# Performance work log

Hardware: AMD Instinct MI355X
Metric: run time of the kernel (lower is better)

## Reference

```python
import jax, jax.numpy as jnp
import numpy as np

L = 4096   # num_tokens (one prefill sequence)
D = 2048   # hidden_size
HK = 16    # num_k_heads
HV = 32    # num_v_heads
DK = 128   # head_k_dim
DV = 128   # head_v_dim
RATIO = HV // HK
EPS = 1e-6


def setup_inputs() -> dict:
    key = jax.random.key(0)
    ks = jax.random.split(key, 11)
    s = 0.02
    return {
        "hidden_states": jax.random.normal(ks[0], (L, D), jnp.float32),
        "Wq": jax.random.normal(ks[1], (D, HK * DK), jnp.float32) * s,
        "Wk": jax.random.normal(ks[2], (D, HK * DK), jnp.float32) * s,
        "Wv": jax.random.normal(ks[3], (D, HV * DV), jnp.float32) * s,
        "Wz": jax.random.normal(ks[4], (D, HV * DV), jnp.float32) * s,
        "Wb": jax.random.normal(ks[5], (D, HV), jnp.float32) * s,
        "Wa": jax.random.normal(ks[6], (D, HV), jnp.float32) * s,
        "A_log": jnp.log(jax.random.uniform(ks[7], (HV,), jnp.float32, 1.0, 16.0)),
        "dt_bias": jax.random.normal(ks[8], (HV,), jnp.float32) * 0.5,
        "norm_weight": jnp.ones((DV,), jnp.float32),
        "W_out": jax.random.normal(ks[9], (HV * DV, D), jnp.float32) * s,
    }


def _l2norm(x):
    return x * jax.lax.rsqrt(jnp.sum(x * x, axis=-1, keepdims=True) + EPS)


def reference(hidden_states, Wq, Wk, Wv, Wz, Wb, Wa, A_log, dt_bias, norm_weight, W_out):
    h = hidden_states
    # --- input projections (qkvz + ba split) ---
    q = _l2norm((h @ Wq).reshape(L, HK, DK))            # [L, HK, DK]
    k = _l2norm((h @ Wk).reshape(L, HK, DK))
    v = (h @ Wv).reshape(L, HV, DV)                     # [L, HV, DV]
    z = (h @ Wz).reshape(L, HV, DV)                     # gate for RMSNorm
    beta = jax.nn.sigmoid(h @ Wb)                       # [L, HV]
    g = -jnp.exp(A_log) * jax.nn.softplus(h @ Wa + dt_bias)  # [L, HV]
    decay = jnp.exp(g)                                  # per-token per-head decay
    # repeat shared q/k heads to value heads (GQA ratio)
    q = jnp.repeat(q, RATIO, axis=1) * (DK ** -0.5)     # [L, HV, DK]
    k = jnp.repeat(k, RATIO, axis=1)

    # --- gated delta rule recurrence over tokens ---
    def step(S, xs):
        q_t, k_t, v_t, b_t, d_t = xs                    # [HV,DK],[HV,DK],[HV,DV],[HV],[HV]
        S = S * d_t[:, None, None]                      # decay state [HV, DK, DV]
        pred = jnp.einsum('hk,hkv->hv', k_t, S)         # memory readout
        delta = (v_t - pred) * b_t[:, None]             # delta-rule correction
        S = S + k_t[:, :, None] * delta[:, None, :]
        o = jnp.einsum('hk,hkv->hv', q_t, S)
        return S, o

    S0 = jnp.zeros((HV, DK, DV), jnp.float32)
    _, core = jax.lax.scan(step, S0, (q, k, v, beta, decay))  # core: [L, HV, DV]

    # --- gated RMSNorm: x * silu(z), rms-normalize over head dim ---
    x = core * jax.nn.silu(z)
    x = x * jax.lax.rsqrt(jnp.mean(x * x, axis=-1, keepdims=True) + EPS) * norm_weight

    # --- output projection ---
    return x.reshape(L, HV * DV) @ W_out                # [L, D]
```

## Files before the change

kernel.cpp:

```cpp
#include <hip/hip_runtime.h>

#define LTOK 4096
#define DHID 2048
#define HKN  16
#define HVN  32
#define DKK  128
#define NTOT 12288

typedef unsigned short u16;
typedef __attribute__((ext_vector_type(8))) short short8;
typedef __attribute__((ext_vector_type(8))) unsigned short u16x8;
typedef __attribute__((ext_vector_type(4))) unsigned short u16x4;
typedef __attribute__((ext_vector_type(4))) float f32x4;

__device__ __forceinline__ float b2f(u16 u) {
  unsigned int x = ((unsigned int)u) << 16;
  return __builtin_bit_cast(float, x);
}
__device__ __forceinline__ u16 f2bf(float f) {
  unsigned int u = __builtin_bit_cast(unsigned int, f);
  u += 0x7FFFu + ((u >> 16) & 1u);
  return (u16)(u >> 16);
}

template<int C> __device__ __forceinline__ float dppmv(float x) {
  int i = __builtin_amdgcn_update_dpp(0, __builtin_bit_cast(int, x), C, 0xF, 0xF, true);
  return __builtin_bit_cast(float, i);
}
__device__ __forceinline__ float red16(float x) {
  x += dppmv<0xB1>(x);
  x += dppmv<0x4E>(x);
  x += dppmv<0x124>(x);
  x += dppmv<0x128>(x);
  return x;
}

__device__ __forceinline__ void gld16(const void* g, void* l) {
  __builtin_amdgcn_global_load_lds((const __attribute__((address_space(1))) void*)g,
                                   (__attribute__((address_space(3))) void*)l, 16, 0, 0);
}

template<int OFF> __device__ __forceinline__ short8 dsr(unsigned a) {
  short8 r;
  asm volatile("ds_read_b128 %0, %1 offset:%2" : "=v"(r) : "v"(a), "n"(OFF));
  return r;
}

__device__ __forceinline__ int sw16(int r, int c, int rowc) { return (r * rowc + c) ^ ((r & 7) << 3); }

__device__ __forceinline__ void cstore(u16* C, size_t i, float v) { C[i] = f2bf(v); }
__device__ __forceinline__ void cstore(float* C, size_t i, float v) { C[i] = v; }

__global__ __launch_bounds__(256)
void k_cvt(const float* __restrict__ s, u16* __restrict__ d, int n) {
  const int i = (blockIdx.x * 256 + threadIdx.x) * 4;
  const float4 v = *(const float4*)(s + i);
  ushort4 o;
  o.x = f2bf(v.x); o.y = f2bf(v.y); o.z = f2bf(v.z); o.w = f2bf(v.w);
  *(ushort4*)(d + i) = o;
}

__global__ __launch_bounds__(256)
void k_tr(const float* __restrict__ src, u16* __restrict__ dst, int R, int C) {
  __shared__ float tl[32][33];
  const int r0 = blockIdx.y * 32, c0 = blockIdx.x * 32;
  const int tr = threadIdx.x >> 3, tc = (threadIdx.x & 7) * 4;
  const float4 v = *(const float4*)(src + (size_t)(r0 + tr) * C + c0 + tc);
  tl[tr][tc] = v.x; tl[tr][tc + 1] = v.y; tl[tr][tc + 2] = v.z; tl[tr][tc + 3] = v.w;
  __syncthreads();
  ushort4 o;
  o.x = f2bf(tl[tc + 0][tr]); o.y = f2bf(tl[tc + 1][tr]);
  o.z = f2bf(tl[tc + 2][tr]); o.w = f2bf(tl[tc + 3][tr]);
  *(ushort4*)(dst + (size_t)(c0 + tr) * R + r0 + tc) = o;
}

#define MFMA16(a, b, c) __builtin_amdgcn_mfma_f32_16x16x32_bf16(a, b, c, 0, 0, 0)

template<typename OutT, int NWN>
__global__ __launch_bounds__(512, 2)
void k_g256(const u16* __restrict__ A, const u16* __restrict__ Bt, OutT* __restrict__ C,
            int M, int N, int K, int NT) {
  constexpr int BUFE = 8192 + NWN * 2048;
  constexpr int BN = NWN * 64;
  __shared__ u16 Lds[4 * BUFE];
  const int tid = threadIdx.x;
  const int lane = tid & 63, w = tid >> 6;
  const int fr = lane & 15, fq = lane >> 4;
  const int wm = (w >> 2) * 128, wn = (w & 3) * (NWN * 16);
  const int nkt = K >> 5;
  const size_t sK = (size_t)K;

  const int MT = gridDim.x / NT;
  const int nts = (NT < 16) ? NT : 16;
  const int per_super = MT * nts;
  const int super = blockIdx.x / per_super;
  const int within = blockIdx.x % per_super;
  const int mtg = MT >> 3;
  const int q = within >> 3;
  const int mt = (within & 7) * mtg + (q % mtg);
  const int nt = super * nts + q / mtg;

  const int kslot = ((tid & 3) ^ ((tid >> 3) & 3)) * 8;
  const u16* aS = A + (size_t)(mt * 256 + (tid >> 2)) * sK + kslot;
  const u16* bS = Bt + (size_t)(nt * BN + (tid >> 2)) * sK + kslot;

  f32x4 acc[8][NWN] = {};

  auto STAGE = [&](int kt_) {
    const int sk = (kt_ < nkt) ? kt_ : nkt - 1;
    u16* base = &Lds[(kt_ & 3) * BUFE];
    gld16(aS + (size_t)sk * 32, base + w * 512);
    gld16(aS + 128 * sK + (size_t)sk * 32, base + w * 512 + 4096);
    gld16(bS + (size_t)sk * 32, base + 8192 + w * 512);
    if constexpr (NWN == 4)
      gld16(bS + 128 * sK + (size_t)sk * 32, base + 8192 + w * 512 + 4096);
  };

  STAGE(0); STAGE(1); STAGE(2);

  const int akey = (fr >> 1) & 3;
  const unsigned ldsBase = (unsigned)(size_t)(__attribute__((address_space(3))) void*)&Lds[0];
  const unsigned aA0 = ldsBase + 2u * (unsigned)((wm + fr) * 32 + ((fq ^ akey) << 3));
  const unsigned bA0 = ldsBase + 2u * (unsigned)(8192 + (wn + fr) * 32 + ((fq ^ akey) << 3));

  for (int kt = 0; kt < nkt; ++kt) {
    if constexpr (NWN == 4) asm volatile("s_waitcnt vmcnt(8)" ::: "memory");
    else                    asm volatile("s_waitcnt vmcnt(6)" ::: "memory");
    __builtin_amdgcn_s_barrier();
    __builtin_amdgcn_sched_barrier(0);
    STAGE(kt + 3);
    const unsigned bo = (unsigned)((kt & 3) * BUFE * 2);
    const unsigned aA = aA0 + bo, bA = bA0 + bo;
    short8 af[8], bf[NWN];
    bf[0] = dsr<0>(bA); bf[1] = dsr<1024>(bA);
    if constexpr (NWN == 4) { bf[2] = dsr<2048>(bA); bf[3] = dsr<3072>(bA); }
    af[0] = dsr<0>(aA);    af[1] = dsr<1024>(aA);
    af[2] = dsr<2048>(aA); af[3] = dsr<3072>(aA);
    af[4] = dsr<4096>(aA); af[5] = dsr<5120>(aA);
    af[6] = dsr<6144>(aA); af[7] = dsr<7168>(aA);
    asm volatile("s_waitcnt lgkmcnt(6)" ::: "memory");
    __builtin_amdgcn_sched_barrier(0);
    __builtin_amdgcn_s_setprio(1);
#pragma unroll
    for (int j = 0; j < NWN; ++j) { acc[0][j] = MFMA16(af[0], bf[j], acc[0][j]);
                                    acc[1][j] = MFMA16(af[1], bf[j], acc[1][j]); }
    asm volatile("s_waitcnt lgkmcnt(4)" ::: "memory");
    __builtin_amdgcn_sched_barrier(0);
#pragma unroll
    for (int j = 0; j < NWN; ++j) { acc[2][j] = MFMA16(af[2], bf[j], acc[2][j]);
                                    acc[3][j] = MFMA16(af[3], bf[j], acc[3][j]); }
    asm volatile("s_waitcnt lgkmcnt(2)" ::: "memory");
    __builtin_amdgcn_sched_barrier(0);
#pragma unroll
    for (int j = 0; j < NWN; ++j) { acc[4][j] = MFMA16(af[4], bf[j], acc[4][j]);
                                    acc[5][j] = MFMA16(af[5], bf[j], acc[5][j]); }
    asm volatile("s_waitcnt lgkmcnt(0)" ::: "memory");
    __builtin_amdgcn_sched_barrier(0);
#pragma unroll
    for (int j = 0; j < NWN; ++j) { acc[6][j] = MFMA16(af[6], bf[j], acc[6][j]);
                                    acc[7][j] = MFMA16(af[7], bf[j], acc[7][j]); }
    __builtin_amdgcn_s_setprio(0);
  }

  const int r0 = mt * 256 + wm + fq * 4;
  const int c0 = nt * BN + wn + fr;
#pragma unroll
  for (int i = 0; i < 8; ++i)
#pragma unroll
    for (int j = 0; j < NWN; ++j)
#pragma unroll
      for (int e = 0; e < 4; ++e)
        cstore(C, (size_t)(r0 + i * 16 + e) * N + c0 + j * 16, acc[i][j][e]);
}

__global__ __launch_bounds__(256)
void k_ba(const float* __restrict__ h, const float* __restrict__ Wb, const float* __restrict__ Wa,
          const float* __restrict__ A_log, const float* __restrict__ dtb,
          float* __restrict__ beta, float* __restrict__ g_out) {
  const int w = threadIdx.x >> 6, lane = threadIdx.x & 63;
  const int t = blockIdx.x * 4 + w;
  const int j = lane & 31;
  const bool isB = lane < 32;
  const float* __restrict__ hr = h + (size_t)t * DHID;
  const float* Wc = isB ? Wb : Wa;
  float acc = 0.f;
  for (int kk = 0; kk < DHID; ++kk) acc = fmaf(hr[kk], Wc[(size_t)kk * HVN + j], acc);
  if (isB) {
    beta[(size_t)t * HVN + j] = 1.f / (1.f + expf(-acc));
  } else {
    float xx = acc + dtb[j];
    float sp = (xx > 20.f) ? xx : log1pf(expf(xx));
    g_out[(size_t)t * HVN + j] = -expf(A_log[j]) * sp;
  }
}

__global__ __launch_bounds__(256)
void k_l2n(u16* __restrict__ qkvz) {
  const int w = threadIdx.x >> 6, lane = threadIdx.x & 63;
  const int r = blockIdx.x * 4 + w;
  const int isK = r >> 16;
  const int rr = r & 65535;
  const int t = rr >> 4, hd = rr & 15;
  u16* p = qkvz + (size_t)t * NTOT + isK * 2048 + hd * DKK + lane * 2;
  float a = b2f(p[0]), b = b2f(p[1]);
  float ss = a * a + b * b;
  ss = red16(ss);
  ss += __shfl_xor(ss, 16);
  ss += __shfl_xor(ss, 32);
  const float sc = rsqrtf(ss + 1e-6f) * (isK ? 1.f : 0.08838834764831845f);
  p[0] = f2bf(a * sc); p[1] = f2bf(b * sc);
}

__global__ __launch_bounds__(256)
void k_r1(const u16* __restrict__ qkvz, const float* __restrict__ beta_g,
          const float* __restrict__ g_g, u16* __restrict__ UM_g, float* __restrict__ cumL_g) {
  const int pair = blockIdx.x;
  const int hv = pair >> 6, n = pair & 63;
  const int hk = hv >> 1;
  const int t0 = n * 64;
  const int tid = threadIdx.x, lane = tid & 63, wv = tid >> 6;
  const int fr = lane & 15, fq = lane >> 4;

  __shared__ __align__(16) u16 Xb[256 * 64];
  __shared__ __align__(16) u16 Dbuf0[64 * 64 * 2];
  __shared__ __align__(16) u16 Dbuf1[64 * 64 * 2];
  __shared__ float Lc[64];
  __shared__ float Bc[64];
  u16* Kl = Dbuf0;

  const int j = tid & 63, h = tid >> 6;
  const u16* kg = qkvz + (size_t)(t0 + j) * NTOT + 2048 + hk * DKK + h * 32;
  const u16* vg = qkvz + (size_t)(t0 + j) * NTOT + 4096 + hv * DKK + h * 32;
  u16x8 kv[4], vv[4];
#pragma unroll
  for (int i = 0; i < 4; ++i) { kv[i] = *(const u16x8*)(kg + i * 8); vv[i] = *(const u16x8*)(vg + i * 8); }
  if (tid < 64) {
    Lc[tid] = g_g[(size_t)(t0 + tid) * HVN + hv];
    Bc[tid] = beta_g[(size_t)(t0 + tid) * HVN + hv];
  }
#pragma unroll
  for (int i = 0; i < 4; ++i) *(u16x8*)&Kl[sw16(j, h * 32 + i * 8, 128)] = kv[i];
  __syncthreads();
  if (tid == 0) { float a = 0.f; for (int t = 0; t < 64; ++t) { a += Lc[t]; Lc[t] = a; } }
  __syncthreads();
  if (tid < 64) cumL_g[(size_t)pair * 64 + tid] = Lc[tid];

  {
    const float bj = Bc[j];
    const float mj = bj * __expf(Lc[j]);
#pragma unroll
    for (int i = 0; i < 4; ++i)
#pragma unroll
      for (int e = 0; e < 8; ++e) {
        int c = h * 32 + i * 8 + e;
        Xb[sw16(c, j, 64)] = f2bf(bj * b2f(vv[i][e]));
        Xb[sw16(128 + c, j, 64)] = f2bf(mj * b2f(kv[i][e]));
      }
  }
  f32x4 kk[4] = {};
#pragma unroll
  for (int ks = 0; ks < 4; ++ks) {
    short8 afr = *(const short8*)&Kl[sw16(wv * 16 + fr, ks * 32 + fq * 8, 128)];
#pragma unroll
    for (int ct = 0; ct < 4; ++ct) {
      short8 bfr = *(const short8*)&Kl[sw16(ct * 16 + fr, ks * 32 + fq * 8, 128)];
      kk[ct] = MFMA16(afr, bfr, kk[ct]);
    }
  }
  __syncthreads();

  f32x4 acc[16];
#pragma unroll
  for (int ct = 0; ct < 16; ++ct) {
    u16x4 xi = *(const u16x4*)&Xb[sw16(ct * 16 + fr, wv * 16 + fq * 4, 64)];
    acc[ct][0] = b2f(xi[0]); acc[ct][1] = b2f(xi[1]); acc[ct][2] = b2f(xi[2]); acc[ct][3] = b2f(xi[3]);
  }
#pragma unroll
  for (int ct = 0; ct < 4; ++ct) {
    const int s = ct * 16 + fr;
    u16x4 pk;
#pragma unroll
    for (int e = 0; e < 4; ++e) {
      const int t = wv * 16 + fq * 4 + e;
      float v = (s < t) ? -Bc[t] * __expf(Lc[t] - Lc[s]) * kk[ct][e] : 0.f;
      pk[e] = f2bf(v);
      Dbuf0[sw16(t, s, 64)] = pk[e];
    }
    *(u16x4*)&Dbuf0[4096 + sw16(s, wv * 16 + fq * 4, 64)] = pk;
  }
  __syncthreads();

  u16* DA = Dbuf0;
  u16* DB = Dbuf1;
  for (int stg = 0; stg < 6; ++stg) {
    u16* Dr = DA;
    u16* Dc = DA + 4096;
    short8 da0 = *(const short8*)&Dr[sw16(wv * 16 + fr, 0 + fq * 8, 64)];
    short8 da1 = *(const short8*)&Dr[sw16(wv * 16 + fr, 32 + fq * 8, 64)];
#pragma unroll
    for (int ct = 0; ct < 16; ++ct) {
      short8 b0 = *(const short8*)&Xb[sw16(ct * 16 + fr, 0 + fq * 8, 64)];
      short8 b1 = *(const short8*)&Xb[sw16(ct * 16 + fr, 32 + fq * 8, 64)];
      acc[ct] = MFMA16(da0, b0, acc[ct]);
      acc[ct] = MFMA16(da1, b1, acc[ct]);
    }
    f32x4 sq[4] = {};
    if (stg < 5) {
#pragma unroll
      for (int ct = 0; ct < 4; ++ct) {
        short8 sb0 = *(const short8*)&Dc[sw16(ct * 16 + fr, 0 + fq * 8, 64)];
        short8 sb1 = *(const short8*)&Dc[sw16(ct * 16 + fr, 32 + fq * 8, 64)];
        sq[ct] = MFMA16(da0, sb0, sq[ct]);
        sq[ct] = MFMA16(da1, sb1, sq[ct]);
      }
    }
    __syncthreads();
#pragma unroll
    for (int ct = 0; ct < 16; ++ct) {
      u16x4 pk;
      pk[0] = f2bf(acc[ct][0]); pk[1] = f2bf(acc[ct][1]); pk[2] = f2bf(acc[ct][2]); pk[3] = f2bf(acc[ct][3]);
      *(u16x4*)&Xb[sw16(ct * 16 + fr, wv * 16 + fq * 4, 64)] = pk;
    }
    if (stg < 5) {
#pragma unroll
      for (int ct = 0; ct < 4; ++ct) {
        u16x4 pk;
        pk[0] = f2bf(sq[ct][0]); pk[1] = f2bf(sq[ct][1]); pk[2] = f2bf(sq[ct][2]); pk[3] = f2bf(sq[ct][3]);
        *(u16x4*)&(DB + 4096)[sw16(ct * 16 + fr, wv * 16 + fq * 4, 64)] = pk;
#pragma unroll
        for (int e = 0; e < 4; ++e) DB[sw16(wv * 16 + fq * 4 + e, ct * 16 + fr, 64)] = pk[e];
      }
    }
    __syncthreads();
    u16* tmp = DA; DA = DB; DB = tmp;
  }

#pragma unroll
  for (int ct = 0; ct < 16; ++ct) {
    const int c = ct * 16 + fr;
#pragma unroll
    for (int e = 0; e < 4; ++e) {
      const int t = wv * 16 + fq * 4 + e;
      float v = acc[ct][e];
      if (ct >= 8) v = -v;
      UM_g[((size_t)pair * 64 + t) * 256 + c] = f2bf(v);
    }
  }
}

__global__ __launch_bounds__(512)
void k_r2(u16* __restrict__ qkvz, const u16* __restrict__ UM_g,
          const float* __restrict__ cumL_g, u16* __restrict__ o1_g) {
  const int hv = blockIdx.x >> 1, cs = blockIdx.x & 1;
  const int hk = hv >> 1;
  const int tid = threadIdx.x, lane = tid & 63, w = tid >> 6;
  const int fr = lane & 15, fq = lane >> 4;
  const int j = tid & 63, h = tid >> 6;

  __shared__ __align__(16) u16 Ml2[2][8192];
  __shared__ __align__(16) u16 Ql2[2][8192];
  __shared__ __align__(16) u16 Kt2[2][8192];
  __shared__ __align__(16) u16 Ul2[2][4096];
  __shared__ __align__(16) u16 dT[4096];
  __shared__ __align__(16) u16 SbT[8192];
  __shared__ __align__(16) u16 o1b[4096];
  __shared__ float Lc2[2][64];

  const int tw = w & 3;
  const int d0 = (w >> 2) * 2;

  f32x4 sacc[4];
#pragma unroll
  for (int d = 0; d < 4; ++d) sacc[d] = (f32x4){0.f, 0.f, 0.f, 0.f};
  for (int i = tid; i < 8192; i += 512) SbT[i] = 0;

  u16x8 pQ0, pQ1, pK0, pK1, pM0, pM1, pU0;
  float pL, pL63;

#define PREF(nn) {                                                            \
    const int nc = ((nn) < 64) ? (nn) : 63;                                   \
    const int pr = hv * 64 + nc; const int tt0 = nc * 64;                     \
    const u16* qg = qkvz + (size_t)(tt0 + j) * NTOT + hk * DKK + h * 16;      \
    pQ0 = *(const u16x8*)qg;          pQ1 = *(const u16x8*)(qg + 8);          \
    pK0 = *(const u16x8*)(qg + 2048); pK1 = *(const u16x8*)(qg + 2056);       \
    const u16* mg = UM_g + ((size_t)pr * 64 + j) * 256;                       \
    pM0 = *(const u16x8*)(mg + 128 + h * 16);                                 \
    pM1 = *(const u16x8*)(mg + 136 + h * 16);                                 \
    pU0 = *(const u16x8*)(mg + cs * 64 + h * 8);                              \
    pL = cumL_g[(size_t)pr * 64 + j]; pL63 = cumL_g[(size_t)pr * 64 + 63]; }

#define STW(b) {                                                              \
    *(u16x8*)&Ql2[b][sw16(j, h * 16, 128)] = pQ0;                             \
    *(u16x8*)&Ql2[b][sw16(j, h * 16 + 8, 128)] = pQ1;                         \
    *(u16x8*)&Ml2[b][sw16(j, h * 16, 128)] = pM0;                             \
    *(u16x8*)&Ml2[b][sw16(j, h * 16 + 8, 128)] = pM1;                         \
    const float scK = __expf(pL63 - pL);                                      \
    _Pragma("unroll")                                                         \
    for (int e = 0; e < 8; ++e) {                                             \
      Kt2[b][sw16(h * 16 + e, j, 64)] = f2bf(scK * b2f(pK0[e]));              \
      Kt2[b][sw16(h * 16 + 8 + e, j, 64)] = f2bf(scK * b2f(pK1[e]));          \
      Ul2[b][sw16(h * 8 + e, j, 64)] = pU0[e];                                \
    }                                                                         \
    if (h == 0) Lc2[b][j] = pL; }

  PREF(0)
  STW(0)
  __syncthreads();

  for (int n = 0; n < 64; ++n) {
    const int cur = n & 1;
    const int pair = hv * 64 + n, t0 = n * 64;
    const float curL63 = pL63;
    PREF(n + 1)

    short8 amf[4], aqf[4];
#pragma unroll
    for (int ks = 0; ks < 4; ++ks) {
      amf[ks] = *(const short8*)&Ml2[cur][sw16(tw * 16 + fr, ks * 32 + fq * 8, 128)];
      aqf[ks] = *(const short8*)&Ql2[cur][sw16(tw * 16 + fr, ks * 32 + fq * 8, 128)];
    }
    float el[4];
#pragma unroll
    for (int e = 0; e < 4; ++e) el[e] = __expf(Lc2[cur][tw * 16 + fq * 4 + e]);
#pragma unroll
    for (int dd = 0; dd < 2; ++dd) {
      const int d = d0 + dd;
      u16x4 uv = *(const u16x4*)&Ul2[cur][sw16(d * 16 + fr, tw * 16 + fq * 4, 64)];
      f32x4 dc;
      dc[0] = b2f(uv[0]); dc[1] = b2f(uv[1]); dc[2] = b2f(uv[2]); dc[3] = b2f(uv[3]);
      f32x4 oc = {};
#pragma unroll
      for (int ks = 0; ks < 4; ++ks) {
        short8 bs = *(const short8*)&SbT[sw16(d * 16 + fr, ks * 32 + fq * 8, 128)];
        dc = MFMA16(amf[ks], bs, dc);
        oc = MFMA16(aqf[ks], bs, oc);
      }
      u16x4 pk;
      pk[0] = f2bf(dc[0]); pk[1] = f2bf(dc[1]); pk[2] = f2bf(dc[2]); pk[3] = f2bf(dc[3]);
      *(u16x4*)&dT[sw16(d * 16 + fr, tw * 16 + fq * 4, 64)] = pk;
#pragma unroll
      for (int e = 0; e < 4; ++e)
        o1b[sw16(tw * 16 + fq * 4 + e, d * 16 + fr, 64)] = f2bf(oc[e] * el[e]);
    }
    __syncthreads();

    {
      const int i = tid * 8;
      u16x8 vd = *(const u16x8*)&dT[i];
      const int f = cs * 4096 + i;
      *(u16x8*)(qkvz + (size_t)(t0 + (f >> 7)) * NTOT + 4096 + hv * DKK + (f & 127)) = vd;
      u16x8 vo = *(const u16x8*)&o1b[i];
      *(u16x8*)(o1_g + (size_t)pair * 8192 + (size_t)(i >> 6) * 128 + cs * 64 + (i & 63)) = vo;
    }
    STW(cur ^ 1)
    {
      const float eC = __expf(curL63);
      short8 ak0 = *(const short8*)&Kt2[cur][sw16(w * 16 + fr, fq * 8, 64)];
      short8 ak1 = *(const short8*)&Kt2[cur][sw16(w * 16 + fr, 32 + fq * 8, 64)];
#pragma unroll
      for (int d = 0; d < 4; ++d) {
        short8 bd0 = *(const short8*)&dT[sw16(d * 16 + fr, fq * 8, 64)];
        short8 bd1 = *(const short8*)&dT[sw16(d * 16 + fr, 32 + fq * 8, 64)];
        f32x4 sa = sacc[d];
#pragma unroll
        for (int e = 0; e < 4; ++e) sa[e] *= eC;
        sa = MFMA16(ak0, bd0, sa);
        sa = MFMA16(ak1, bd1, sa);
        sacc[d] = sa;
        u16x4 pk;
        pk[0] = f2bf(sa[0]); pk[1] = f2bf(sa[1]); pk[2] = f2bf(sa[2]); pk[3] = f2bf(sa[3]);
        *(u16x4*)&SbT[sw16(d * 16 + fr, w * 16 + fq * 4, 128)] = pk;
      }
    }
    __syncthreads();
  }
#undef PREF
#undef STW
}

__global__ __launch_bounds__(512)
void k_r3(const u16* __restrict__ qkvz, const u16* __restrict__ o1_g,
          const float* __restrict__ cumL_g, const float* __restrict__ nw,
          u16* __restrict__ x) {
  const int pair = blockIdx.x, hv = pair >> 6, n = pair & 63, hk = hv >> 1, t0 = n * 64;
  const int tid = threadIdx.x, lane = tid & 63, w = tid >> 6;
  const int fr = lane & 15, fq = lane >> 4;
  const int j = tid & 63, h = tid >> 6;

  __shared__ __align__(16) u16 Ql[8192];
  __shared__ __align__(16) u16 Kl[8192];
  __shared__ __align__(16) u16 Gl[4096];
  __shared__ __align__(16) u16 dTl[8192];
  __shared__ __align__(16) float of[64 * 132];
  __shared__ float Lc[64];
  __shared__ float Lw[128];

  {
    const u16* qg = qkvz + (size_t)(t0 + j) * NTOT + hk * DKK + h * 16;
    u16x8 q0 = *(const u16x8*)qg, q1 = *(const u16x8*)(qg + 8);
    u16x8 k0 = *(const u16x8*)(qg + 2048), k1 = *(const u16x8*)(qg + 2056);
    *(u16x8*)&Ql[sw16(j, h * 16, 128)] = q0;
    *(u16x8*)&Ql[sw16(j, h * 16 + 8, 128)] = q1;
    *(u16x8*)&Kl[sw16(j, h * 16, 128)] = k0;
    *(u16x8*)&Kl[sw16(j, h * 16 + 8, 128)] = k1;
  }
#pragma unroll
  for (int it = 0; it < 2; ++it) {
    const int f = ((w * 2 + it) * 64 + lane) * 8;
    gld16(qkvz + (size_t)(t0 + (f >> 7)) * NTOT + 4096 + hv * DKK + (f & 127),
          (char*)dTl + (w * 2 + it) * 1024);
  }
  if (tid < 64) Lc[tid] = cumL_g[(size_t)pair * 64 + tid];
  if (tid < 128) Lw[tid] = nw[tid];
  __syncthreads();

  const int tw = w & 3, sp = (w >> 2) * 2;
  {
    f32x4 kk0 = {}, kk1 = {};
#pragma unroll
    for (int ks = 0; ks < 4; ++ks) {
      short8 aq = *(const short8*)&Ql[sw16(tw * 16 + fr, ks * 32 + fq * 8, 128)];
      short8 b0 = *(const short8*)&Kl[sw16(sp * 16 + fr, ks * 32 + fq * 8, 128)];
      short8 b1 = *(const short8*)&Kl[sw16((sp + 1) * 16 + fr, ks * 32 + fq * 8, 128)];
      kk0 = MFMA16(aq, b0, kk0);
      kk1 = MFMA16(aq, b1, kk1);
    }
#pragma unroll
    for (int e = 0; e < 4; ++e) {
      const int t = tw * 16 + fq * 4 + e;
      const float Lt = Lc[t];
      const int s0 = sp * 16 + fr, s1 = s0 + 16;
      Gl[sw16(t, s0, 64)] = f2bf((s0 <= t) ? kk0[e] * __expf(Lt - Lc[s0]) : 0.f);
      Gl[sw16(t, s1, 64)] = f2bf((s1 <= t) ? kk1[e] * __expf(Lt - Lc[s1]) : 0.f);
    }
  }
  __syncthreads();

  {
    short8 ag0 = *(const short8*)&Gl[sw16(tw * 16 + fr, fq * 8, 64)];
    short8 ag1 = *(const short8*)&Gl[sw16(tw * 16 + fr, 32 + fq * 8, 64)];
#pragma unroll
    for (int dd = 0; dd < 4; ++dd) {
      const int d = (w >> 2) * 4 + dd;
      short8 bd0 = *(const short8*)&dTl[sw16(d * 16 + fr, fq * 8, 64)];
      short8 bd1 = *(const short8*)&dTl[sw16(d * 16 + fr, 32 + fq * 8, 64)];
      f32x4 oc = {};
      oc = MFMA16(ag0, bd0, oc);
      oc = MFMA16(ag1, bd1, oc);
#pragma unroll
      for (int e = 0; e < 4; ++e) of[(tw * 16 + fq * 4 + e) * 132 + d * 16 + fr] = oc[e];
    }
  }
  __syncthreads();

  {
    const int t = tid >> 3, q8 = tid & 7;
    const u16* zp = qkvz + (size_t)(t0 + t) * NTOT + 8192 + hv * DKK + q8 * 16;
    const u16* op = o1_g + (size_t)pair * 8192 + t * 128;
    float xv[16];
    float ss = 0.f;
#pragma unroll
    for (int i = 0; i < 2; ++i) {
      u16x8 zv = *(const u16x8*)(zp + i * 8);
      u16x8 ov = *(const u16x8*)(op + (((q8 * 16 + i * 8) ^ ((t & 7) << 3))));
#pragma unroll
      for (int e = 0; e < 8; ++e) {
        float z = b2f(zv[e]);
        float o = of[t * 132 + q8 * 16 + i * 8 + e] + b2f(ov[e]);
        float xx = o * (z / (1.f + __expf(-z)));
        xv[i * 8 + e] = xx;
        ss = fmaf(xx, xx, ss);
      }
    }
    ss += __shfl_xor(ss, 1);
    ss += __shfl_xor(ss, 2);
    ss += __shfl_xor(ss, 4);
    const float scl = rsqrtf(ss * (1.f / 128.f) + 1e-6f);
    u16* xo = x + (size_t)(t0 + t) * 4096 + hv * DKK + q8 * 16;
#pragma unroll
    for (int i = 0; i < 2; ++i) {
      u16x8 pk;
#pragma unroll
      for (int e = 0; e < 8; ++e) pk[e] = f2bf(xv[i * 8 + e] * scl * Lw[q8 * 16 + i * 8 + e]);
      *(u16x8*)(xo + i * 8) = pk;
    }
  }
}

extern "C" void kernel_launch(void* const* d_in, const int* in_sizes, int n_in,
                              void* d_out, int out_size, void* d_ws, size_t ws_size,
                              hipStream_t stream) {
  const float* h    = (const float*)d_in[0];
  const float* Wq   = (const float*)d_in[1];
  const float* Wk   = (const float*)d_in[2];
  const float* Wv   = (const float*)d_in[3];
  const float* Wz   = (const float*)d_in[4];
  const float* Wb   = (const float*)d_in[5];
  const float* Wa   = (const float*)d_in[6];
  const float* Alog = (const float*)d_in[7];
  const float* dtb  = (const float*)d_in[8];
  const float* nw   = (const float*)d_in[9];
  const float* Wo   = (const float*)d_in[10];
  char* ws = (char*)d_ws;
  u16* h_bf  = (u16*)(ws);
  u16* Wt    = (u16*)(ws + 16777216ull);
  u16* UM    = (u16*)(ws);
  u16* Wto   = (u16*)(ws + 67108864ull);
  u16* qkvz  = (u16*)(ws + 83886080ull);
  u16* o1g   = (u16*)(ws + 184549376ull);
  u16* xbuf  = (u16*)(ws + 16777216ull);
  float* beta  = (float*)(ws + 218103808ull);
  float* g     = (float*)(ws + 218103808ull + 524288ull);
  float* cumL  = (float*)(ws + 218103808ull + 1048576ull);

  k_cvt<<<8192, 256, 0, stream>>>(h, h_bf, LTOK * DHID);
  k_tr<<<dim3(64, 64), 256, 0, stream>>>(Wq, Wt, 2048, 2048);
  k_tr<<<dim3(64, 64), 256, 0, stream>>>(Wk, Wt + 2048ull * 2048, 2048, 2048);
  k_tr<<<dim3(128, 64), 256, 0, stream>>>(Wv, Wt + 4096ull * 2048, 2048, 4096);
  k_tr<<<dim3(128, 64), 256, 0, stream>>>(Wz, Wt + 8192ull * 2048, 2048, 4096);
  k_tr<<<dim3(64, 128), 256, 0, stream>>>(Wo, Wto, 4096, 2048);
  k_g256<u16, 4><<<768, 512, 0, stream>>>(h_bf, Wt, qkvz, 4096, 12288, 2048, 48);
  k_ba<<<1024, 256, 0, stream>>>(h, Wb, Wa, Alog, dtb, beta, g);
  k_l2n<<<32768, 256, 0, stream>>>(qkvz);
  k_r1<<<2048, 256, 0, stream>>>(qkvz, beta, g, UM, cumL);
  k_r2<<<64, 512, 0, stream>>>(qkvz, UM, cumL, o1g);
  k_r3<<<2048, 512, 0, stream>>>(qkvz, o1g, cumL, nw, xbuf);
  k_g256<float, 2><<<256, 512, 0, stream>>>(xbuf, Wto, (float*)d_out, 4096, 2048, 4096, 16);
}
```

Measured before the change: 831.3 us.

## Split sequential recurrence kernel across four value-column slices per head

```diff
diff --git a/kernel.cpp b/kernel.cpp
--- a/kernel.cpp
+++ b/kernel.cpp
@@ -351,30 +351,28 @@
 __global__ __launch_bounds__(512)
 void k_r2(u16* __restrict__ qkvz, const u16* __restrict__ UM_g,
           const float* __restrict__ cumL_g, u16* __restrict__ o1_g) {
-  const int hv = blockIdx.x >> 1, cs = blockIdx.x & 1;
+  const int hv = blockIdx.x >> 2, cs = blockIdx.x & 3;
   const int hk = hv >> 1;
   const int tid = threadIdx.x, lane = tid & 63, w = tid >> 6;
   const int fr = lane & 15, fq = lane >> 4;
   const int j = tid & 63, h = tid >> 6;
+  const int tw = w & 3, dwv = w >> 2;
 
   __shared__ __align__(16) u16 Ml2[2][8192];
   __shared__ __align__(16) u16 Ql2[2][8192];
   __shared__ __align__(16) u16 Kt2[2][8192];
-  __shared__ __align__(16) u16 Ul2[2][4096];
-  __shared__ __align__(16) u16 dT[4096];
-  __shared__ __align__(16) u16 SbT[8192];
-  __shared__ __align__(16) u16 o1b[4096];
+  __shared__ __align__(16) u16 dT[2048];
+  __shared__ __align__(16) u16 SbT[4096];
+  __shared__ __align__(16) u16 o1b[2048];
   __shared__ float Lc2[2][64];
 
-  const int tw = w & 3;
-  const int d0 = (w >> 2) * 2;
-
-  f32x4 sacc[4];
-#pragma unroll
-  for (int d = 0; d < 4; ++d) sacc[d] = (f32x4){0.f, 0.f, 0.f, 0.f};
-  for (int i = tid; i < 8192; i += 512) SbT[i] = 0;
-
-  u16x8 pQ0, pQ1, pK0, pK1, pM0, pM1, pU0;
+  f32x4 sacc[2];
+#pragma unroll
+  for (int d = 0; d < 2; ++d) sacc[d] = (f32x4){0.f, 0.f, 0.f, 0.f};
+  for (int i = tid; i < 4096; i += 512) SbT[i] = 0;
+
+  u16x8 pQ0, pQ1, pK0, pK1, pM0, pM1;
+  u16 pUn0, pUn1, pUn2, pUn3, pUc0, pUc1, pUc2, pUc3;
   float pL, pL63;
 
 #define PREF(nn) {                                                            \
@@ -386,7 +384,9 @@
     const u16* mg = UM_g + ((size_t)pr * 64 + j) * 256;                       \
     pM0 = *(const u16x8*)(mg + 128 + h * 16);                                 \
     pM1 = *(const u16x8*)(mg + 136 + h * 16);                                 \
-    pU0 = *(const u16x8*)(mg + cs * 64 + h * 8);                              \
+    const u16* ug = UM_g + ((size_t)pr * 64 + tw * 16 + fq * 4) * 256         \
+                    + cs * 32 + dwv * 16 + fr;                                \
+    pUn0 = ug[0]; pUn1 = ug[256]; pUn2 = ug[512]; pUn3 = ug[768];             \
     pL = cumL_g[(size_t)pr * 64 + j]; pL63 = cumL_g[(size_t)pr * 64 + 63]; }
 
 #define STW(b) {                                                              \
@@ -399,7 +399,6 @@
     for (int e = 0; e < 8; ++e) {                                             \
       Kt2[b][sw16(h * 16 + e, j, 64)] = f2bf(scK * b2f(pK0[e]));              \
       Kt2[b][sw16(h * 16 + 8 + e, j, 64)] = f2bf(scK * b2f(pK1[e]));          \
-      Ul2[b][sw16(h * 8 + e, j, 64)] = pU0[e];                                \
     }                                                                         \
     if (h == 0) Lc2[b][j] = pL; }
 
@@ -410,6 +409,7 @@
   for (int n = 0; n < 64; ++n) {
     const int cur = n & 1;
     const int pair = hv * 64 + n, t0 = n * 64;
+    pUc0 = pUn0; pUc1 = pUn1; pUc2 = pUn2; pUc3 = pUn3;
     const float curL63 = pL63;
     PREF(n + 1)
 
@@ -422,35 +422,33 @@
     float el[4];
 #pragma unroll
     for (int e = 0; e < 4; ++e) el[e] = __expf(Lc2[cur][tw * 16 + fq * 4 + e]);
-#pragma unroll
-    for (int dd = 0; dd < 2; ++dd) {
-      const int d = d0 + dd;
-      u16x4 uv = *(const u16x4*)&Ul2[cur][sw16(d * 16 + fr, tw * 16 + fq * 4, 64)];
+    {
       f32x4 dc;
-      dc[0] = b2f(uv[0]); dc[1] = b2f(uv[1]); dc[2] = b2f(uv[2]); dc[3] = b2f(uv[3]);
+      dc[0] = b2f(pUc0); dc[1] = b2f(pUc1); dc[2] = b2f(pUc2); dc[3] = b2f(pUc3);
       f32x4 oc = {};
 #pragma unroll
       for (int ks = 0; ks < 4; ++ks) {
-        short8 bs = *(const short8*)&SbT[sw16(d * 16 + fr, ks * 32 + fq * 8, 128)];
+        short8 bs = *(const short8*)&SbT[sw16(dwv * 16 + fr, ks * 32 + fq * 8, 128)];
         dc = MFMA16(amf[ks], bs, dc);
         oc = MFMA16(aqf[ks], bs, oc);
       }
-      u16x4 pk;
-      pk[0] = f2bf(dc[0]); pk[1] = f2bf(dc[1]); pk[2] = f2bf(dc[2]); pk[3] = f2bf(dc[3]);
-      *(u16x4*)&dT[sw16(d * 16 + fr, tw * 16 + fq * 4, 64)] = pk;
-#pragma unroll
-      for (int e = 0; e < 4; ++e)
-        o1b[sw16(tw * 16 + fq * 4 + e, d * 16 + fr, 64)] = f2bf(oc[e] * el[e]);
+      u16x4 pkd;
+      pkd[0] = f2bf(dc[0]); pkd[1] = f2bf(dc[1]); pkd[2] = f2bf(dc[2]); pkd[3] = f2bf(dc[3]);
+      *(u16x4*)&dT[sw16(dwv * 16 + fr, tw * 16 + fq * 4, 64)] = pkd;
+      u16x4 pko;
+#pragma unroll
+      for (int e = 0; e < 4; ++e) pko[e] = f2bf(oc[e] * el[e]);
+      *(u16x4*)&o1b[sw16(dwv * 16 + fr, tw * 16 + fq * 4, 64)] = pko;
     }
     __syncthreads();
 
     {
-      const int i = tid * 8;
-      u16x8 vd = *(const u16x8*)&dT[i];
-      const int f = cs * 4096 + i;
-      *(u16x8*)(qkvz + (size_t)(t0 + (f >> 7)) * NTOT + 4096 + hv * DKK + (f & 127)) = vd;
-      u16x8 vo = *(const u16x8*)&o1b[i];
-      *(u16x8*)(o1_g + (size_t)pair * 8192 + (size_t)(i >> 6) * 128 + cs * 64 + (i & 63)) = vo;
+      const int i = tid * 4;
+      u16x4 vd = *(const u16x4*)&dT[i];
+      const int f = cs * 2048 + i;
+      *(u16x4*)(qkvz + (size_t)(t0 + (f >> 7)) * NTOT + 4096 + hv * DKK + (f & 127)) = vd;
+      u16x4 vo = *(const u16x4*)&o1b[i];
+      *(u16x4*)(o1_g + (size_t)pair * 8192 + cs * 2048 + i) = vo;
     }
     STW(cur ^ 1)
     {
@@ -458,7 +456,7 @@
       short8 ak0 = *(const short8*)&Kt2[cur][sw16(w * 16 + fr, fq * 8, 64)];
       short8 ak1 = *(const short8*)&Kt2[cur][sw16(w * 16 + fr, 32 + fq * 8, 64)];
 #pragma unroll
-      for (int d = 0; d < 4; ++d) {
+      for (int d = 0; d < 2; ++d) {
         short8 bd0 = *(const short8*)&dT[sw16(d * 16 + fr, fq * 8, 64)];
         short8 bd1 = *(const short8*)&dT[sw16(d * 16 + fr, 32 + fq * 8, 64)];
         f32x4 sa = sacc[d];
@@ -491,6 +489,7 @@
   __shared__ __align__(16) u16 Kl[8192];
   __shared__ __align__(16) u16 Gl[4096];
   __shared__ __align__(16) u16 dTl[8192];
+  __shared__ __align__(16) u16 o1l[8192];
   __shared__ __align__(16) float of[64 * 132];
   __shared__ float Lc[64];
   __shared__ float Lw[128];
@@ -509,6 +508,7 @@
     const int f = ((w * 2 + it) * 64 + lane) * 8;
     gld16(qkvz + (size_t)(t0 + (f >> 7)) * NTOT + 4096 + hv * DKK + (f & 127),
           (char*)dTl + (w * 2 + it) * 1024);
+    gld16(o1_g + (size_t)pair * 8192 + f, (char*)o1l + (w * 2 + it) * 1024);
   }
   if (tid < 64) Lc[tid] = cumL_g[(size_t)pair * 64 + tid];
   if (tid < 128) Lw[tid] = nw[tid];
@@ -556,17 +556,16 @@
   {
     const int t = tid >> 3, q8 = tid & 7;
     const u16* zp = qkvz + (size_t)(t0 + t) * NTOT + 8192 + hv * DKK + q8 * 16;
-    const u16* op = o1_g + (size_t)pair * 8192 + t * 128;
     float xv[16];
     float ss = 0.f;
 #pragma unroll
     for (int i = 0; i < 2; ++i) {
       u16x8 zv = *(const u16x8*)(zp + i * 8);
-      u16x8 ov = *(const u16x8*)(op + (((q8 * 16 + i * 8) ^ ((t & 7) << 3))));
 #pragma unroll
       for (int e = 0; e < 8; ++e) {
+        const int dv = q8 * 16 + i * 8 + e;
         float z = b2f(zv[e]);
-        float o = of[t * 132 + q8 * 16 + i * 8 + e] + b2f(ov[e]);
+        float o = of[t * 132 + dv] + b2f(o1l[sw16(dv, t, 64)]);
         float xx = o * (z / (1.f + __expf(-z)));
         xv[i * 8 + e] = xx;
         ss = fmaf(xx, xx, ss);
@@ -623,7 +622,7 @@
   k_ba<<<1024, 256, 0, stream>>>(h, Wb, Wa, Alog, dtb, beta, g);
   k_l2n<<<32768, 256, 0, stream>>>(qkvz);
   k_r1<<<2048, 256, 0, stream>>>(qkvz, beta, g, UM, cumL);
-  k_r2<<<64, 512, 0, stream>>>(qkvz, UM, cumL, o1g);
+  k_r2<<<128, 512, 0, stream>>>(qkvz, UM, cumL, o1g);
   k_r3<<<2048, 512, 0, stream>>>(qkvz, o1g, cumL, nw, xbuf);
   k_g256<float, 2><<<256, 512, 0, stream>>>(xbuf, Wto, (float*)d_out, 4096, 2048, 4096, 16);
 }
```

Result: faster. 812.4 us (-2.3%).
